# Optimization experiments

Hardware: AMD Instinct MI355X
Metric: run time of the kernel (lower is better)

Reference implementation:

```python
import jax, jax.numpy as jnp
import numpy as np

N_HEAD = 4
D_K = 512 // N_HEAD  # 128
PAD = 5  # (kernel 11 - 1) // 2, sanm_shift=0 -> symmetric 'same' padding
EPS = 1e-5


def layer_norm(x, w, b):
    m = jnp.mean(x, axis=-1, keepdims=True)
    v = jnp.mean(jnp.square(x - m), axis=-1, keepdims=True)
    return (x - m) * jax.lax.rsqrt(v + EPS) * w + b


def setup_inputs() -> dict:
    key = jax.random.key(0)
    ks = jax.random.split(key, 8)
    B, T, D = 64, 218, 512
    s = 0.05
    return {
        "x": jax.random.normal(ks[0], (B, T, D), jnp.float32),
        "masks": jnp.ones((B, T), jnp.float32),
        "ln0_w": jax.random.uniform(ks[1], (D,), jnp.float32, 0.9, 1.1),
        "ln0_b": jnp.zeros((D,), jnp.float32),
        "ln1_w": jax.random.uniform(ks[2], (D,), jnp.float32, 0.9, 1.1),
        "ln1_b": jnp.zeros((D,), jnp.float32),
        "qkv_w": jax.random.normal(ks[3], (D, 3 * D), jnp.float32) * s,
        "qkv_b": jnp.zeros((3 * D,), jnp.float32),
        "out_w": jax.random.normal(ks[4], (D, D), jnp.float32) * s,
        "out_b": jnp.zeros((D,), jnp.float32),
        "fsmn_w": jax.random.normal(ks[5], (D, D, 11), jnp.float32) * s,
        "w1": jax.random.normal(ks[6], (D, 4 * D), jnp.float32) * s,
        "b1": jnp.zeros((4 * D,), jnp.float32),
        "w2": jax.random.normal(ks[7], (4 * D, D), jnp.float32) * s,
        "b2": jnp.zeros((D,), jnp.float32),
    }


def encoder_layer(x, masks, ln0_w, ln0_b, ln1_w, ln1_b, qkv_w, qkv_b,
                  out_w, out_b, fsmn_w, w1, b1, w2, b2):
    B, T, D = x.shape
    m = masks[..., None]  # (B,T,1)

    # ---- self_attn_sanm block ----
    residual = x
    h = layer_norm(x, ln0_w, ln0_b)
    qkv = h @ qkv_w + qkv_b                      # (B,T,3D)
    q, k, v = jnp.split(qkv, 3, axis=-1)         # each (B,T,D)

    # FSMN memory branch on (masked) v: Conv1d(512,512,11), 'same' padding
    vm = v * m
    # torch conv weight (out,in,k) -> jax 'WIO' kernel (k,in,out)
    kern = jnp.transpose(fsmn_w, (2, 1, 0))
    fsmn = jax.lax.conv_general_dilated(
        vm, kern, window_strides=(1,), padding=[(PAD, PAD)],
        dimension_numbers=("NWC", "WIO", "NWC"))
    fsmn = (fsmn + vm) * m                       # (B,T,D)

    # multi-head attention
    def heads(t):  # (B,T,D) -> (B,H,T,dk)
        return t.reshape(B, T, N_HEAD, D_K).transpose(0, 2, 1, 3)
    qh, kh, vh = heads(q), heads(k), heads(v)
    scores = jnp.einsum("bhqd,bhkd->bhqk", qh, kh) / np.sqrt(D_K)
    neg = jnp.finfo(scores.dtype).min
    scores = jnp.where(masks[:, None, None, :] > 0, scores, neg)
    attn = jax.nn.softmax(scores, axis=-1)
    ctx = jnp.einsum("bhqk,bhkd->bhqd", attn, vh)
    ctx = ctx.transpose(0, 2, 1, 3).reshape(B, T, D)
    att_out = ctx @ out_w + out_b + fsmn
    x = residual + att_out

    # ---- feed-forward block (512 -> 2048 -> 512, relu) ----
    residual = x
    h = layer_norm(x, ln1_w, ln1_b)
    ffn = jax.nn.relu(h @ w1 + b1) @ w2 + b2
    return residual + ffn


def reference(x, masks, ln0_w, ln0_b, ln1_w, ln1_b, qkv_w, qkv_b,
              out_w, out_b, fsmn_w, w1, b1, w2, b2):
    return encoder_layer(x, masks, ln0_w, ln0_b, ln1_w, ln1_b,
                         qkv_w, qkv_b, out_w, out_b, fsmn_w, w1, b1, w2, b2)
```

## Files before the change

kernel.cpp:

```cpp
#include <hip/hip_runtime.h>
#include <cstdint>

#define B_   64
#define T_   218
#define TP_  228
#define D_   512
#define M_   13952
#define MT_  109
#define H_   4
#define DK_  128
#define N3_  1536
#define DFF_ 2048
#define KC_  5632

typedef unsigned short u16;
using short8 = __attribute__((ext_vector_type(8))) short;
using f32x4  = __attribute__((ext_vector_type(4))) float;

__device__ __forceinline__ float b2f(u16 u) {
  union { float f; uint32_t i; } v; v.i = ((uint32_t)u) << 16; return v.f;
}
__device__ __forceinline__ u16 f2b(float f) {
  union { float f; uint32_t i; } v; v.f = f;
  uint32_t r = v.i + 0x7fffu + ((v.i >> 16) & 1u);
  return (u16)(r >> 16);
}
union U8 { uint4 v; u16 u[8]; };

__device__ __forceinline__ void gll16(const u16* g, u16* l) {
  __builtin_amdgcn_global_load_lds(
      (const __attribute__((address_space(1))) unsigned int*)g,
      (__attribute__((address_space(3))) unsigned int*)l, 16, 0, 0);
}

template<int MODE>
__global__ __launch_bounds__(256, 2)
void gemm_u(const u16* __restrict__ A, int sA, const u16* __restrict__ Bt, int sB,
            const float* __restrict__ bias, const u16* __restrict__ convb,
            u16* __restrict__ vmout,
            const float* __restrict__ add_f, void* __restrict__ outp,
            int N, int K, int ntc, const float* __restrict__ masks)
{
  __shared__ u16 As[128 * 32];
  __shared__ u16 Bs[128 * 32];

  const int xcd = blockIdx.x & 7;
  const int lin = blockIdx.x >> 3;
  const int nt = lin % ntc;
  const int mt = xcd + 8 * (lin / ntc);
  if (mt >= MT_) return;
  const int m0 = mt * 128, n0 = nt * 128;

  const int tid = threadIdx.x, lane = tid & 63, w = tid >> 6;
  const int wm = (w >> 1) * 64, wn = (w & 1) * 64;
  const int l15 = lane & 15, qd = lane >> 4;

  const int rl = lane >> 2, ce = (lane & 3) * 8;
  const int r0 = m0 + w * 16 + rl, r1 = r0 + 64;
  const u16* ag0 = A + (size_t)r0 * sA + ce;
  const u16* ag1 = A + (size_t)r1 * sA + ce;
  const u16* bg0 = Bt + (size_t)(n0 + w * 16 + rl) * sB + ce;
  const u16* bg1 = bg0 + (size_t)64 * sB;
  u16* lA0 = As + w * 512;
  u16* lA1 = As + 2048 + w * 512;
  u16* lB0 = Bs + w * 512;
  u16* lB1 = Bs + 2048 + w * 512;

  const f32x4 z4 = {0.f, 0.f, 0.f, 0.f};
  f32x4 acc[4][4];
#pragma unroll
  for (int i = 0; i < 4; i++)
#pragma unroll
    for (int j = 0; j < 4; j++) acc[i][j] = z4;

  for (int k0 = 0; k0 < K; k0 += 32) {
    __syncthreads();
    gll16(ag0 + k0, lA0);
    gll16(ag1 + k0, lA1);
    gll16(bg0 + k0, lB0);
    gll16(bg1 + k0, lB1);
    __syncthreads();
    short8 af[4], bf[4];
#pragma unroll
    for (int mi = 0; mi < 4; mi++) af[mi] = *(const short8*)&As[(wm + mi * 16 + l15) * 32 + qd * 8];
#pragma unroll
    for (int ni = 0; ni < 4; ni++) bf[ni] = *(const short8*)&Bs[(wn + ni * 16 + l15) * 32 + qd * 8];
#pragma unroll
    for (int mi = 0; mi < 4; mi++)
#pragma unroll
      for (int ni = 0; ni < 4; ni++)
        acc[mi][ni] = __builtin_amdgcn_mfma_f32_16x16x32_bf16(af[mi], bf[ni], acc[mi][ni], 0, 0, 0);
  }

#pragma unroll
  for (int ni = 0; ni < 4; ni++) {
    const int c = n0 + wn + ni * 16 + l15;
    const float bv = bias[c];
#pragma unroll
    for (int mi = 0; mi < 4; mi++) {
#pragma unroll
      for (int rg = 0; rg < 4; rg++) {
        const int r = m0 + wm + mi * 16 + qd * 4 + rg;
        float v = acc[mi][ni][rg] + bv;
        if (MODE == 0) {
          ((u16*)outp)[(size_t)r * N + c] = f2b(v);
          if (c >= 1024) {
            const int b = r / T_, t = r - b * T_;
            vmout[((size_t)b * TP_ + t + 5) * D_ + (c - 1024)] = f2b(v * masks[r]);
          }
        } else if (MODE == 1) {
          const size_t idx = (size_t)r * N + c;
          ((float*)outp)[idx] = v + b2f(convb[idx]) + add_f[idx];
        } else if (MODE == 2) {
          ((u16*)outp)[(size_t)r * N + c] = f2b(fmaxf(v, 0.f));
        } else {
          const size_t idx = (size_t)r * N + c;
          ((float*)outp)[idx] = v + add_f[idx];
        }
      }
    }
  }
}

__global__ __launch_bounds__(256, 2)
void conv_gemm(const u16* __restrict__ vmpad, const u16* __restrict__ Wt,
               const float* __restrict__ masks, u16* __restrict__ convb)
{
  __shared__ u16 As[288 * 32];
  __shared__ u16 Bs[11 * 64 * 32];

  const int nt = blockIdx.x & 7, mt = blockIdx.x >> 3;
  const int m0 = mt * 256, n0 = nt * 64;
  const int b0 = m0 / T_;
  const int base = m0 + 10 * b0;

  const int tid = threadIdx.x, lane = tid & 63, w = tid >> 6;
  const int wm = (w >> 1) * 128, wn = (w & 1) * 32;
  const int l15 = lane & 15, qd = lane >> 4;
  const int rl = lane >> 2, ce = (lane & 3) * 8;

  int arow[8];
#pragma unroll
  for (int mi = 0; mi < 8; mi++) {
    const int mo = wm + mi * 16 + l15;
    const int db = (m0 + mo) / T_ - b0;
    arow[mi] = mo + 10 * db;
  }

  const f32x4 z4 = {0.f, 0.f, 0.f, 0.f};
  f32x4 acc[8][2];
#pragma unroll
  for (int i = 0; i < 8; i++) { acc[i][0] = z4; acc[i][1] = z4; }

  for (int kc = 0; kc < 16; kc++) {
    const int kb = kc * 32;
    __syncthreads();
    for (int c = w; c < 18; c += 4)
      gll16(vmpad + (size_t)(base + c * 16 + rl) * D_ + kb + ce, As + c * 512);
    for (int c = w; c < 44; c += 4) {
      const int tap = c >> 2, q = c & 3;
      gll16(Wt + (size_t)(n0 + q * 16 + rl) * KC_ + tap * 512 + kb + ce,
            Bs + c * 512);
    }
    __syncthreads();
#pragma unroll
    for (int tap = 0; tap < 11; tap++) {
      short8 bf0 = *(const short8*)&Bs[tap * 2048 + (wn + l15) * 32 + qd * 8];
      short8 bf1 = *(const short8*)&Bs[tap * 2048 + (wn + 16 + l15) * 32 + qd * 8];
#pragma unroll
      for (int mi = 0; mi < 8; mi++) {
        short8 af = *(const short8*)&As[(arow[mi] + tap) * 32 + qd * 8];
        acc[mi][0] = __builtin_amdgcn_mfma_f32_16x16x32_bf16(af, bf0, acc[mi][0], 0, 0, 0);
        acc[mi][1] = __builtin_amdgcn_mfma_f32_16x16x32_bf16(af, bf1, acc[mi][1], 0, 0, 0);
      }
    }
  }

#pragma unroll
  for (int mi = 0; mi < 8; mi++) {
#pragma unroll
    for (int rg = 0; rg < 4; rg++) {
      const int r = m0 + wm + mi * 16 + qd * 4 + rg;
      if (r < M_) {
        const int b = r / T_;
        const int vrow = r + 10 * b + 5;
        const float m = masks[r];
#pragma unroll
        for (int ni = 0; ni < 2; ni++) {
          const int c = n0 + wn + ni * 16 + l15;
          const float vm = b2f(vmpad[(size_t)vrow * D_ + c]);
          convb[(size_t)r * D_ + c] = f2b((acc[mi][ni][rg] + vm) * m);
        }
      }
    }
  }
}

__global__ __launch_bounds__(256, 2)
void attn_fused(const u16* __restrict__ qkv, const float* __restrict__ masks,
                u16* __restrict__ ctx)
{
  __shared__ u16 smem[29696];
  __shared__ float red0[4][64];
  __shared__ float red1[4][64];
  u16* Qs = smem;
  u16* Ks = smem + 64 * 136;
  u16* Ps = smem;
  u16* Vs = smem + 64 * 232;

  const int tid = threadIdx.x, lane = tid & 63, w = tid >> 6;
  const int l15 = lane & 15, qd = lane >> 4;
  const int bh = blockIdx.y, b = bh >> 2, h = bh & 3;
  const int q0 = blockIdx.x * 64;
  const uint4 uz = make_uint4(0, 0, 0, 0);

#pragma unroll
  for (int i = 0; i < 4; i++) {
    const int ch = tid + i * 256;
    const int row = ch >> 4, cg = (ch & 15) * 8;
    const int t = q0 + row;
    uint4 v = uz;
    if (t < T_) v = *(const uint4*)(qkv + ((size_t)b * T_ + t) * N3_ + h * DK_ + cg);
    *(uint4*)&Qs[row * 136 + cg] = v;
  }

  const f32x4 z4 = {0.f, 0.f, 0.f, 0.f};
  f32x4 acc[4][4];
#pragma unroll
  for (int i = 0; i < 4; i++)
#pragma unroll
    for (int j = 0; j < 4; j++) acc[i][j] = z4;

#pragma unroll
  for (int kc = 0; kc < 4; kc++) {
    __syncthreads();
#pragma unroll
    for (int i = 0; i < 4; i++) {
      const int ch = tid + i * 256;
      const int row = ch >> 4, cg = (ch & 15) * 8;
      const int t = kc * 64 + row;
      uint4 v = uz;
      if (t < T_) v = *(const uint4*)(qkv + ((size_t)b * T_ + t) * N3_ + D_ + h * DK_ + cg);
      *(uint4*)&Ks[row * 136 + cg] = v;
    }
    __syncthreads();
#pragma unroll
    for (int ks = 0; ks < 4; ks++) {
      short8 bf = *(const short8*)&Ks[(w * 16 + l15) * 136 + ks * 32 + qd * 8];
#pragma unroll
      for (int mi = 0; mi < 4; mi++) {
        short8 af = *(const short8*)&Qs[(mi * 16 + l15) * 136 + ks * 32 + qd * 8];
        acc[kc][mi] = __builtin_amdgcn_mfma_f32_16x16x32_bf16(af, bf, acc[kc][mi], 0, 0, 0);
      }
    }
  }

  const float scale = 0.08838834764831845f;
  const int colb = w * 16 + l15;
  bool valid[4];
#pragma unroll
  for (int kc = 0; kc < 4; kc++) {
    const int col = kc * 64 + colb;
    valid[kc] = (col < T_) && (masks[b * T_ + col] > 0.f);
  }

  float mx[4][4];
#pragma unroll
  for (int mi = 0; mi < 4; mi++)
#pragma unroll
    for (int rg = 0; rg < 4; rg++) {
      float m = -1e30f;
#pragma unroll
      for (int kc = 0; kc < 4; kc++)
        if (valid[kc]) m = fmaxf(m, acc[kc][mi][rg] * scale);
      for (int d = 1; d < 16; d <<= 1) m = fmaxf(m, __shfl_xor(m, d, 64));
      mx[mi][rg] = m;
    }
  if (l15 == 0) {
#pragma unroll
    for (int mi = 0; mi < 4; mi++)
#pragma unroll
      for (int rg = 0; rg < 4; rg++) red0[w][mi * 16 + qd * 4 + rg] = mx[mi][rg];
  }
  __syncthreads();
#pragma unroll
  for (int mi = 0; mi < 4; mi++)
#pragma unroll
    for (int rg = 0; rg < 4; rg++) {
      const int r = mi * 16 + qd * 4 + rg;
      mx[mi][rg] = fmaxf(fmaxf(red0[0][r], red0[1][r]), fmaxf(red0[2][r], red0[3][r]));
    }
  float sm[4][4];
#pragma unroll
  for (int mi = 0; mi < 4; mi++)
#pragma unroll
    for (int rg = 0; rg < 4; rg++) {
      float s = 0.f;
#pragma unroll
      for (int kc = 0; kc < 4; kc++)
        if (valid[kc]) s += __expf(acc[kc][mi][rg] * scale - mx[mi][rg]);
      for (int d = 1; d < 16; d <<= 1) s += __shfl_xor(s, d, 64);
      sm[mi][rg] = s;
    }
  if (l15 == 0) {
#pragma unroll
    for (int mi = 0; mi < 4; mi++)
#pragma unroll
      for (int rg = 0; rg < 4; rg++) red1[w][mi * 16 + qd * 4 + rg] = sm[mi][rg];
  }
  __syncthreads();
#pragma unroll
  for (int mi = 0; mi < 4; mi++)
#pragma unroll
    for (int rg = 0; rg < 4; rg++) {
      const int r = mi * 16 + qd * 4 + rg;
      const float inv = 1.f / (red1[0][r] + red1[1][r] + red1[2][r] + red1[3][r]);
#pragma unroll
      for (int kc = 0; kc < 4; kc++) {
        const int col = kc * 64 + colb;
        if (col < 224) {
          const float p = valid[kc] ? __expf(acc[kc][mi][rg] * scale - mx[mi][rg]) * inv : 0.f;
          Ps[r * 232 + col] = f2b(p);
        }
      }
    }

  const int kvg = tid >> 4, dg = tid & 15;
#pragma unroll
  for (int half = 0; half < 2; ++half) {
    __syncthreads();
#pragma unroll
    for (int r = 0; r < 14; ++r) {
      const int kv = r * 16 + kvg;
      ushort4 vv = make_ushort4(0, 0, 0, 0);
      if (kv < T_)
        vv = *(const ushort4*)(qkv + ((size_t)b * T_ + kv) * N3_ + 1024 + h * DK_ + half * 64 + dg * 4);
      Vs[(dg * 4 + 0) * 232 + kv] = vv.x;
      Vs[(dg * 4 + 1) * 232 + kv] = vv.y;
      Vs[(dg * 4 + 2) * 232 + kv] = vv.z;
      Vs[(dg * 4 + 3) * 232 + kv] = vv.w;
    }
    __syncthreads();
    f32x4 a2[4] = {z4, z4, z4, z4};
#pragma unroll
    for (int k0 = 0; k0 < 7; ++k0) {
      short8 af = *(const short8*)&Ps[(w * 16 + l15) * 232 + k0 * 32 + qd * 8];
#pragma unroll
      for (int nt = 0; nt < 4; ++nt) {
        short8 bf = *(const short8*)&Vs[(nt * 16 + l15) * 232 + k0 * 32 + qd * 8];
        a2[nt] = __builtin_amdgcn_mfma_f32_16x16x32_bf16(af, bf, a2[nt], 0, 0, 0);
      }
    }
    const int tb = q0 + w * 16 + qd * 4;
#pragma unroll
    for (int nt = 0; nt < 4; ++nt) {
      const int d = h * DK_ + half * 64 + nt * 16 + l15;
#pragma unroll
      for (int rg = 0; rg < 4; ++rg) {
        const int tt = tb + rg;
        if (tt < T_) ctx[((size_t)b * T_ + tt) * D_ + d] = f2b(a2[nt][rg]);
      }
    }
  }
}

__global__ __launch_bounds__(256)
void ln_k(const float* __restrict__ x, const float* __restrict__ wgt,
          const float* __restrict__ bia, u16* __restrict__ outp)
{
  const int lane = threadIdx.x & 63, wv = threadIdx.x >> 6;
  const size_t row = (size_t)blockIdx.x * 4 + wv;
  const float* rp = x + row * D_ + lane * 8;
  float v[8], s = 0.f, s2 = 0.f;
  float4 r0 = *(const float4*)rp;
  float4 r1 = *(const float4*)(rp + 4);
  v[0] = r0.x; v[1] = r0.y; v[2] = r0.z; v[3] = r0.w;
  v[4] = r1.x; v[5] = r1.y; v[6] = r1.z; v[7] = r1.w;
#pragma unroll
  for (int i = 0; i < 8; i++) { s += v[i]; s2 += v[i] * v[i]; }
  for (int d = 1; d < 64; d <<= 1) { s += __shfl_xor(s, d, 64); s2 += __shfl_xor(s2, d, 64); }
  const float mean = s * (1.f / 512.f);
  const float var  = s2 * (1.f / 512.f) - mean * mean;
  const float rs   = rsqrtf(var + 1e-5f);
  float4 w0 = *(const float4*)(wgt + lane * 8);
  float4 w1 = *(const float4*)(wgt + lane * 8 + 4);
  float4 b0 = *(const float4*)(bia + lane * 8);
  float4 b1 = *(const float4*)(bia + lane * 8 + 4);
  const float wv8[8] = {w0.x, w0.y, w0.z, w0.w, w1.x, w1.y, w1.z, w1.w};
  const float bv8[8] = {b0.x, b0.y, b0.z, b0.w, b1.x, b1.y, b1.z, b1.w};
  U8 o;
#pragma unroll
  for (int i = 0; i < 8; i++)
    o.u[i] = f2b((v[i] - mean) * rs * wv8[i] + bv8[i]);
  *(uint4*)(outp + row * D_ + lane * 8) = o.v;
}

__global__ __launch_bounds__(256)
void prep_all(const float* __restrict__ qkv_w, const float* __restrict__ out_w,
              const float* __restrict__ w1, const float* __restrict__ w2,
              const float* __restrict__ fsmn_w,
              u16* __restrict__ qkv_wT, u16* __restrict__ out_wT,
              u16* __restrict__ w1T, u16* __restrict__ w2T,
              u16* __restrict__ fsmnW2, u16* __restrict__ vmpad)
{
  const int bid = blockIdx.x;
  if (bid < 3072) {
    const float* src; u16* dst; int K, N, tb;
    if (bid < 768)       { src = qkv_w; dst = qkv_wT; K = 512;  N = 1536; tb = bid; }
    else if (bid < 1024) { src = out_w; dst = out_wT; K = 512;  N = 512;  tb = bid - 768; }
    else if (bid < 2048) { src = w1;    dst = w1T;    K = 512;  N = 2048; tb = bid - 1024; }
    else                 { src = w2;    dst = w2T;    K = 2048; N = 512;  tb = bid - 2048; }
    const int ktiles = K / 32;
    const int k0 = (tb % ktiles) * 32, n0 = (tb / ktiles) * 32;
    __shared__ float tile[32][33];
    const int x = threadIdx.x & 31, y = threadIdx.x >> 5;
#pragma unroll
    for (int j = 0; j < 4; j++)
      tile[y + j * 8][x] = src[(size_t)(k0 + y + j * 8) * N + n0 + x];
    __syncthreads();
#pragma unroll
    for (int j = 0; j < 4; j++)
      dst[(size_t)(n0 + y + j * 8) * K + k0 + x] = f2b(tile[x][y + j * 8]);
  } else if (bid < 4096) {
    const int idx = (bid - 3072) * 256 + threadIdx.x;
    const int o = idx >> 9, i = idx & 511;
    const float* s = fsmn_w + (size_t)idx * 11;
#pragma unroll
    for (int tap = 0; tap < 11; ++tap)
      fsmnW2[(size_t)o * KC_ + tap * 512 + i] = f2b(s[tap]);
  } else {
    const int e8 = (bid - 4096) * 256 + threadIdx.x;
    const int e  = e8 * 8;
    const int c  = e & 511;
    const int pr = e >> 9;
    int row;
    if (pr < 640) {
      const int b = pr / 10, j = pr % 10;
      row = b * TP_ + ((j < 5) ? j : (218 + j));
    } else {
      row = B_ * TP_ + (pr - 640);
    }
    *(uint4*)(vmpad + (size_t)row * D_ + c) = make_uint4(0, 0, 0, 0);
  }
}

extern "C" void kernel_launch(void* const* d_in, const int* in_sizes, int n_in,
                              void* d_out, int out_size, void* d_ws, size_t ws_size,
                              hipStream_t stream)
{
  const float* x      = (const float*)d_in[0];
  const float* masks  = (const float*)d_in[1];
  const float* ln0_w  = (const float*)d_in[2];
  const float* ln0_b  = (const float*)d_in[3];
  const float* ln1_w  = (const float*)d_in[4];
  const float* ln1_b  = (const float*)d_in[5];
  const float* qkv_w  = (const float*)d_in[6];
  const float* qkv_b  = (const float*)d_in[7];
  const float* out_w  = (const float*)d_in[8];
  const float* out_b  = (const float*)d_in[9];
  const float* fsmn_w = (const float*)d_in[10];
  const float* w1     = (const float*)d_in[11];
  const float* b1     = (const float*)d_in[12];
  const float* w2     = (const float*)d_in[13];
  const float* b2     = (const float*)d_in[14];
  float* outp = (float*)d_out;
  u16* ws   = (u16*)d_ws;

  size_t off = 0;
  u16* qkv_wT = ws + off; off += (size_t)1536 * 512;
  u16* out_wT = ws + off; off += (size_t)512 * 512;
  u16* w1T    = ws + off; off += (size_t)2048 * 512;
  u16* w2T    = ws + off; off += (size_t)512 * 2048;
  u16* fsmnW2 = ws + off; off += (size_t)512 * KC_;
  u16* slotA  = ws + off; off += (size_t)M_ * 512;
  u16* qkvb   = ws + off; off += (size_t)M_ * 1536;
  u16* vmpad  = ws + off; off += (size_t)(B_ * TP_ + 320) * 512;
  u16* regionX= ws + off;
  u16* convb  = regionX;
  u16* hid    = regionX;
  u16* h1     = qkvb;
  float* x1   = (float*)(qkvb + (size_t)M_ * 512);

  prep_all<<<4126, 256, 0, stream>>>(qkv_w, out_w, w1, w2, fsmn_w,
                                     qkv_wT, out_wT, w1T, w2T, fsmnW2, vmpad);
  ln_k<<<M_ / 4, 256, 0, stream>>>(x, ln0_w, ln0_b, slotA);
  gemm_u<0><<<8 * 14 * 12, 256, 0, stream>>>(
      slotA, 512, qkv_wT, 512, qkv_b, nullptr, vmpad, nullptr, qkvb,
      1536, 512, 12, masks);
  conv_gemm<<<55 * 8, 256, 0, stream>>>(vmpad, fsmnW2, masks, convb);
  attn_fused<<<dim3(4, 256), 256, 0, stream>>>(qkvb, masks, slotA);
  gemm_u<1><<<8 * 14 * 4, 256, 0, stream>>>(
      slotA, 512, out_wT, 512, out_b, convb, nullptr, x, x1,
      512, 512, 4, masks);
  ln_k<<<M_ / 4, 256, 0, stream>>>(x1, ln1_w, ln1_b, h1);
  gemm_u<2><<<8 * 14 * 16, 256, 0, stream>>>(
      h1, 512, w1T, 512, b1, nullptr, nullptr, nullptr, hid,
      2048, 512, 16, nullptr);
  gemm_u<3><<<8 * 14 * 4, 256, 0, stream>>>(
      hid, 2048, w2T, 2048, b2, nullptr, nullptr, x1, outp,
      512, 2048, 4, nullptr);
}
```

Before: 458.2 us.

## Swizzle LDS tiles in GEMMs and retile conv GEMM per batch sequence

Applies an XOR swizzle to the column chunk that global_load_lds writes and the MFMA fragment reads use, in both gemm_u and conv_gemm, to cut LDS bank conflicts. conv_gemm is also retiled so each block handles one batch's 218 padded rows (7 m-subtiles of 16 per warp row) instead of 256 rows that cross batch boundaries. This removes the per-row batch-offset division and wasted padded rows, and launches 512 blocks. The swizzled tap offsets in conv_gemm depend on the row-plus-tap index, which adds index arithmetic and risks subtle addressing errors.

```diff
diff --git a/kernel.cpp b/kernel.cpp
--- a/kernel.cpp
+++ b/kernel.cpp
@@ -33,6 +33,7 @@
       (__attribute__((address_space(3))) unsigned int*)l, 16, 0, 0);
 }
 
+
 template<int MODE>
 __global__ __launch_bounds__(256, 2)
 void gemm_u(const u16* __restrict__ A, int sA, const u16* __restrict__ Bt, int sB,
@@ -55,7 +56,9 @@
   const int wm = (w >> 1) * 64, wn = (w & 1) * 64;
   const int l15 = lane & 15, qd = lane >> 4;
 
-  const int rl = lane >> 2, ce = (lane & 3) * 8;
+  const int rl = lane >> 2;
+  const int ce = ((lane & 3) ^ ((lane >> 3) & 3)) * 8;
+  const int sw8 = (qd ^ ((lane >> 1) & 3)) * 8;
   const int r0 = m0 + w * 16 + rl, r1 = r0 + 64;
   const u16* ag0 = A + (size_t)r0 * sA + ce;
   const u16* ag1 = A + (size_t)r1 * sA + ce;
@@ -82,9 +85,9 @@
     __syncthreads();
     short8 af[4], bf[4];
 #pragma unroll
-    for (int mi = 0; mi < 4; mi++) af[mi] = *(const short8*)&As[(wm + mi * 16 + l15) * 32 + qd * 8];
-#pragma unroll
-    for (int ni = 0; ni < 4; ni++) bf[ni] = *(const short8*)&Bs[(wn + ni * 16 + l15) * 32 + qd * 8];
+    for (int mi = 0; mi < 4; mi++) af[mi] = *(const short8*)&As[(wm + mi * 16 + l15) * 32 + sw8];
+#pragma unroll
+    for (int ni = 0; ni < 4; ni++) bf[ni] = *(const short8*)&Bs[(wn + ni * 16 + l15) * 32 + sw8];
 #pragma unroll
     for (int mi = 0; mi < 4; mi++)
 #pragma unroll
@@ -126,36 +129,37 @@
 void conv_gemm(const u16* __restrict__ vmpad, const u16* __restrict__ Wt,
                const float* __restrict__ masks, u16* __restrict__ convb)
 {
-  __shared__ u16 As[288 * 32];
+  __shared__ u16 As[240 * 32];
   __shared__ u16 Bs[11 * 64 * 32];
 
-  const int nt = blockIdx.x & 7, mt = blockIdx.x >> 3;
-  const int m0 = mt * 256, n0 = nt * 64;
-  const int b0 = m0 / T_;
-  const int base = m0 + 10 * b0;
+  const int nt = blockIdx.x & 7, b = blockIdx.x >> 3;
+  const int n0 = nt * 64;
+  const int base = b * TP_;
 
   const int tid = threadIdx.x, lane = tid & 63, w = tid >> 6;
-  const int wm = (w >> 1) * 128, wn = (w & 1) * 32;
+  const int wm = (w >> 1) * 112, wn = (w & 1) * 32;
   const int l15 = lane & 15, qd = lane >> 4;
-  const int rl = lane >> 2, ce = (lane & 3) * 8;
-
-  int arow[8];
-#pragma unroll
-  for (int mi = 0; mi < 8; mi++) {
-    const int mo = wm + mi * 16 + l15;
-    const int db = (m0 + mo) / T_ - b0;
-    arow[mi] = mo + 10 * db;
-  }
+  const int rl = lane >> 2;
+  const int ce = ((lane & 3) ^ ((lane >> 3) & 3)) * 8;
+
+  int abase[7];
+#pragma unroll
+  for (int mi = 0; mi < 7; mi++) abase[mi] = (wm + mi * 16 + l15) * 64;
+  int toff[11];
+#pragma unroll
+  for (int tap = 0; tap < 11; tap++)
+    toff[tap] = tap * 64 + ((qd ^ (((l15 + tap) >> 1) & 3)) << 4);
+  const int swb8 = (qd ^ ((l15 >> 1) & 3)) * 8;
 
   const f32x4 z4 = {0.f, 0.f, 0.f, 0.f};
-  f32x4 acc[8][2];
-#pragma unroll
-  for (int i = 0; i < 8; i++) { acc[i][0] = z4; acc[i][1] = z4; }
+  f32x4 acc[7][2];
+#pragma unroll
+  for (int i = 0; i < 7; i++) { acc[i][0] = z4; acc[i][1] = z4; }
 
   for (int kc = 0; kc < 16; kc++) {
     const int kb = kc * 32;
     __syncthreads();
-    for (int c = w; c < 18; c += 4)
+    for (int c = w; c < 15; c += 4)
       gll16(vmpad + (size_t)(base + c * 16 + rl) * D_ + kb + ce, As + c * 512);
     for (int c = w; c < 44; c += 4) {
       const int tap = c >> 2, q = c & 3;
@@ -163,13 +167,14 @@
             Bs + c * 512);
     }
     __syncthreads();
+    const char* Ab = (const char*)As;
 #pragma unroll
     for (int tap = 0; tap < 11; tap++) {
-      short8 bf0 = *(const short8*)&Bs[tap * 2048 + (wn + l15) * 32 + qd * 8];
-      short8 bf1 = *(const short8*)&Bs[tap * 2048 + (wn + 16 + l15) * 32 + qd * 8];
-#pragma unroll
-      for (int mi = 0; mi < 8; mi++) {
-        short8 af = *(const short8*)&As[(arow[mi] + tap) * 32 + qd * 8];
+      short8 bf0 = *(const short8*)&Bs[tap * 2048 + (wn + l15) * 32 + swb8];
+      short8 bf1 = *(const short8*)&Bs[tap * 2048 + (wn + 16 + l15) * 32 + swb8];
+#pragma unroll
+      for (int mi = 0; mi < 7; mi++) {
+        short8 af = *(const short8*)(Ab + (abase[mi] + toff[tap]));
         acc[mi][0] = __builtin_amdgcn_mfma_f32_16x16x32_bf16(af, bf0, acc[mi][0], 0, 0, 0);
         acc[mi][1] = __builtin_amdgcn_mfma_f32_16x16x32_bf16(af, bf1, acc[mi][1], 0, 0, 0);
       }
@@ -177,13 +182,13 @@
   }
 
 #pragma unroll
-  for (int mi = 0; mi < 8; mi++) {
+  for (int mi = 0; mi < 7; mi++) {
 #pragma unroll
     for (int rg = 0; rg < 4; rg++) {
-      const int r = m0 + wm + mi * 16 + qd * 4 + rg;
-      if (r < M_) {
-        const int b = r / T_;
-        const int vrow = r + 10 * b + 5;
+      const int rlcl = wm + mi * 16 + qd * 4 + rg;
+      if (rlcl < T_) {
+        const int r = b * T_ + rlcl;
+        const int vrow = base + rlcl + 5;
         const float m = masks[r];
 #pragma unroll
         for (int ni = 0; ni < 2; ni++) {
@@ -487,7 +492,7 @@
   gemm_u<0><<<8 * 14 * 12, 256, 0, stream>>>(
       slotA, 512, qkv_wT, 512, qkv_b, nullptr, vmpad, nullptr, qkvb,
       1536, 512, 12, masks);
-  conv_gemm<<<55 * 8, 256, 0, stream>>>(vmpad, fsmnW2, masks, convb);
+  conv_gemm<<<512, 256, 0, stream>>>(vmpad, fsmnW2, masks, convb);
   attn_fused<<<dim3(4, 256), 256, 0, stream>>>(qkvb, masks, slotA);
   gemm_u<1><<<8 * 14 * 4, 256, 0, stream>>>(
       slotA, 512, out_wT, 512, out_b, convb, nullptr, x, x1,
```

New measurement: 443.6 us. 1.03x faster.
